# Kernel optimization log

Hardware: AMD Instinct MI355X
Metric: run time of the kernel (lower is better)

Reference implementation:

```python
import jax, jax.numpy as jnp
import numpy as np

B, S, D_IN, D_EMB = 16, 8192, 256, 256
LEVELS = 8  # pywt default max level for db1 with signal length 256: log2(256)
INV_SQRT2 = np.float32(1.0 / np.sqrt(2.0))


def haar_wavedec_concat(x, levels):
    """Multi-level Haar (db1) DWT along last axis; returns coeffs concatenated
    in pywt order [cA_L, cD_L, ..., cD_1]. Assumes last dim = 2**levels,
    so 'symmetric' padding is a no-op (filter length 2, even lengths).
    pywt db1 convention: cA[k]=(x[2k]+x[2k+1])/sqrt2, cD[k]=(x[2k]-x[2k+1])/sqrt2.
    """
    details = []
    a = x
    for _ in range(levels):
        even = a[..., ::2]
        odd = a[..., 1::2]
        details.append((even - odd) * INV_SQRT2)
        a = (even + odd) * INV_SQRT2
    return jnp.concatenate([a] + details[::-1], axis=-1)


def setup_inputs() -> dict:
    key = jax.random.key(0)
    k_x, k_w, k_b = jax.random.split(key, 3)
    x = jax.random.normal(k_x, (B, S, D_IN), dtype=jnp.float32)
    # nn.Linear(input_dim, embed_dim): W is (embed_dim, input_dim)
    bound = np.float32(1.0 / np.sqrt(D_IN))
    W = jax.random.uniform(k_w, (D_EMB, D_IN), dtype=jnp.float32, minval=-bound, maxval=bound)
    b = jax.random.uniform(k_b, (D_EMB,), dtype=jnp.float32, minval=-bound, maxval=bound)
    return {"x": x, "W": W, "b": b}


def reference(x, W, b):
    coeffs = haar_wavedec_concat(x, LEVELS)  # (B, S, D_IN)
    # concatenated coeff length == D_IN exactly, so no pad/trim (matches original no-op branch)
    return jnp.einsum('bsd,ed->bse', coeffs, W) + b
```

## Files before the change

### kernel.cpp

```cpp
#include <hip/hip_runtime.h>
#include <hip/hip_bf16.h>

typedef short short8 __attribute__((ext_vector_type(8)));
typedef float f32x4 __attribute__((ext_vector_type(4)));

#define INV_SQRT2F 0.70710678118654752440f

__device__ __forceinline__ unsigned short f2bf(float f) {
  union { float f; unsigned u; } v; v.f = f;
  unsigned u = v.u;
  unsigned r = (u + 0x7FFFu + ((u >> 16) & 1u)) >> 16;
  return (unsigned short)r;
}

__global__ void haar_pack(const float* __restrict__ W, unsigned short* __restrict__ Wp) {
  __shared__ float cbuf[4][256];
  __shared__ float buf0[4][256];
  __shared__ float buf1[4][256];
  const int tid = threadIdx.x;
  const int w = tid >> 6, l = tid & 63;
  const int e = blockIdx.x * 4 + w;
  const float* row = W + e * 256;
  for (int k = l; k < 256; k += 64) cbuf[w][k] = row[k];
  __syncthreads();
  if (l == 0) buf0[w][0] = cbuf[w][0];
  __syncthreads();
  float* A = buf0[w];
  float* Bv = buf1[w];
  int len = 1;
  for (int s = 0; s < 8; ++s) {
    for (int k = l; k < len; k += 64) {
      float av = A[k], dv = cbuf[w][len + k];
      Bv[2 * k]     = (av + dv) * INV_SQRT2F;
      Bv[2 * k + 1] = (av - dv) * INV_SQRT2F;
    }
    __syncthreads();
    float* t = A; A = Bv; Bv = t;
    len <<= 1;
  }
  const int nblk = e >> 4, lr = e & 15;
  for (int k = l; k < 256; k += 64) {
    int kk = k >> 5, win = k & 31, lhi = win >> 3, j = win & 7;
    int lane = lhi * 16 + lr;
    Wp[(((nblk * 8 + kk) * 64 + lane) << 3) + j] = f2bf(A[k]);
  }
}

#define NTILES 16
#define BM 32

#define BARRIER_LGKM() do { \
    __builtin_amdgcn_sched_barrier(0); \
    asm volatile("s_waitcnt lgkmcnt(0)" ::: "memory"); \
    __builtin_amdgcn_s_barrier(); \
    __builtin_amdgcn_sched_barrier(0); \
  } while (0)

__global__ __launch_bounds__(512, 1) void wemb_gemm(
    const float* __restrict__ x, const unsigned short* __restrict__ Wp,
    const float* __restrict__ bias, float* __restrict__ out) {
  __shared__ char al[2][16384];
  const int tid = threadIdx.x;
  const int w = tid >> 6, lane = tid & 63;
  const int wm = w >> 2, wn = w & 3;
  const int lr = lane & 15, lhi = lane >> 4;

  short8 Bf[8][4];
#pragma unroll
  for (int kk = 0; kk < 8; ++kk)
#pragma unroll
    for (int n = 0; n < 4; ++n)
      Bf[kk][n] = *(const short8*)(Wp + ((((wn * 4 + n) * 8 + kk) * 64 + lane) << 3));
#pragma unroll
  for (int kk = 0; kk < 8; ++kk)
#pragma unroll
    for (int n = 0; n < 4; ++n)
      asm volatile("" : "+v"(Bf[kk][n]));

  float bv[4];
#pragma unroll
  for (int n = 0; n < 4; ++n) bv[n] = bias[wn * 64 + n * 16 + lr];

  const long tile0 = (long)blockIdx.x * NTILES;
  float4 pfA[4], pfB[4];

  {
    const float4* s0 = (const float4*)(x + tile0 * (BM * 256));
    float4 t0[4];
#pragma unroll
    for (int i = 0; i < 4; ++i) t0[i] = s0[i * 512 + tid];
    const float4* s1 = (const float4*)(x + (tile0 + 1) * (BM * 256));
#pragma unroll
    for (int i = 0; i < 4; ++i) pfA[i] = s1[i * 512 + tid];
#pragma unroll
    for (int i = 0; i < 4; ++i) {
      int f = i * 512 + tid;
      int row = f >> 6, colb = (f & 63) * 8;
      ushort4 p;
      p.x = __bfloat16_as_ushort(__float2bfloat16(t0[i].x));
      p.y = __bfloat16_as_ushort(__float2bfloat16(t0[i].y));
      p.z = __bfloat16_as_ushort(__float2bfloat16(t0[i].z));
      p.w = __bfloat16_as_ushort(__float2bfloat16(t0[i].w));
      *(ushort4*)(al[0] + row * 512 + (colb ^ ((row & 7) << 4))) = p;
    }
  }
  BARRIER_LGKM();

#define STEP(IT, CUR, NXT, PFU, PFL)                                          \
  {                                                                           \
    const long tt = tile0 + (IT);                                             \
    if ((IT) + 2 < NTILES) {                                                  \
      const float4* src = (const float4*)(x + (tt + 2) * (BM * 256));         \
      _Pragma("unroll")                                                       \
      for (int i = 0; i < 4; ++i) PFL[i] = src[i * 512 + tid];                \
    }                                                                         \
    f32x4 acc[4];                                                             \
    _Pragma("unroll")                                                         \
    for (int n = 0; n < 4; ++n) acc[n] = (f32x4){0.f, 0.f, 0.f, 0.f};         \
    _Pragma("unroll")                                                         \
    for (int kk = 0; kk < 8; ++kk) {                                          \
      const int arow = wm * 16 + lr;                                          \
      const int colb = (kk * 32 + lhi * 8) * 2;                               \
      short8 a = *(const short8*)((CUR) + arow * 512 +                        \
                                  (colb ^ ((arow & 7) << 4)));                \
      _Pragma("unroll")                                                       \
      for (int n = 0; n < 4; ++n)                                             \
        acc[n] = __builtin_amdgcn_mfma_f32_16x16x32_bf16(a, Bf[kk][n],        \
                                                         acc[n], 0, 0, 0);    \
    }                                                                         \
    {                                                                         \
      float* orow = out + (tt * BM + wm * 16 + lhi * 4) * 256;                \
      _Pragma("unroll")                                                       \
      for (int n = 0; n < 4; ++n) {                                           \
        const int e = wn * 64 + n * 16 + lr;                                  \
        _Pragma("unroll")                                                     \
        for (int r = 0; r < 4; ++r) orow[r * 256 + e] = acc[n][r] + bv[n];    \
      }                                                                       \
    }                                                                         \
    if ((IT) + 1 < NTILES) {                                                  \
      _Pragma("unroll")                                                       \
      for (int i = 0; i < 4; ++i) {                                           \
        int f = i * 512 + tid;                                                \
        int row = f >> 6, colb = (f & 63) * 8;                                \
        ushort4 p;                                                            \
        p.x = __bfloat16_as_ushort(__float2bfloat16(PFU[i].x));               \
        p.y = __bfloat16_as_ushort(__float2bfloat16(PFU[i].y));               \
        p.z = __bfloat16_as_ushort(__float2bfloat16(PFU[i].z));               \
        p.w = __bfloat16_as_ushort(__float2bfloat16(PFU[i].w));               \
        *(ushort4*)((NXT) + row * 512 + (colb ^ ((row & 7) << 4))) = p;       \
      }                                                                       \
      BARRIER_LGKM();                                                         \
    }                                                                         \
  }

#pragma unroll 1
  for (int ip = 0; ip < NTILES / 2; ++ip) {
    const int it0 = ip * 2;
    STEP(it0,     al[0], al[1], pfA, pfB);
    STEP(it0 + 1, al[1], al[0], pfB, pfA);
  }
#undef STEP
}

extern "C" void kernel_launch(void* const* d_in, const int* in_sizes, int n_in,
                              void* d_out, int out_size, void* d_ws, size_t ws_size,
                              hipStream_t stream) {
  const float* x = (const float*)d_in[0];
  const float* W = (const float*)d_in[1];
  const float* b = (const float*)d_in[2];
  float* out = (float*)d_out;
  unsigned short* Wp = (unsigned short*)d_ws;

  haar_pack<<<64, 256, 0, stream>>>(W, Wp);

  const int grid = (out_size / 256) / (BM * NTILES);
  wemb_gemm<<<grid, 512, 0, stream>>>(x, Wp, b, out);
}
```

Before: 57.94 us.

## Compute Haar-transformed weights in closed form and double GEMM occupancy

The weight pre-transform kernel replaces the iterative shared-memory inverse-Haar loop with a direct closed-form sum per output element, one thread per element and one block per row, removing the barriers. The GEMM halves tiles per block (doubling grid size) and raises launch bounds to two blocks per CU, dropping the asm register pin on the B fragments. This aims to hide memory latency through more resident waves, at the risk of register pressure or spills from holding 32 B fragments under a tighter register budget.

```diff
diff --git a/kernel.cpp b/kernel.cpp
--- a/kernel.cpp
+++ b/kernel.cpp
@@ -3,8 +3,6 @@
 
 typedef short short8 __attribute__((ext_vector_type(8)));
 typedef float f32x4 __attribute__((ext_vector_type(4)));
-
-#define INV_SQRT2F 0.70710678118654752440f
 
 __device__ __forceinline__ unsigned short f2bf(float f) {
   union { float f; unsigned u; } v; v.f = f;
@@ -14,39 +12,26 @@
 }
 
 __global__ void haar_pack(const float* __restrict__ W, unsigned short* __restrict__ Wp) {
-  __shared__ float cbuf[4][256];
-  __shared__ float buf0[4][256];
-  __shared__ float buf1[4][256];
-  const int tid = threadIdx.x;
-  const int w = tid >> 6, l = tid & 63;
-  const int e = blockIdx.x * 4 + w;
+  const int e = blockIdx.x;
+  const int k = threadIdx.x;
   const float* row = W + e * 256;
-  for (int k = l; k < 256; k += 64) cbuf[w][k] = row[k];
-  __syncthreads();
-  if (l == 0) buf0[w][0] = cbuf[w][0];
-  __syncthreads();
-  float* A = buf0[w];
-  float* Bv = buf1[w];
-  int len = 1;
-  for (int s = 0; s < 8; ++s) {
-    for (int k = l; k < len; k += 64) {
-      float av = A[k], dv = cbuf[w][len + k];
-      Bv[2 * k]     = (av + dv) * INV_SQRT2F;
-      Bv[2 * k + 1] = (av - dv) * INV_SQRT2F;
-    }
-    __syncthreads();
-    float* t = A; A = Bv; Bv = t;
-    len <<= 1;
+  const float wgt[9] = {0.f,
+    0.70710678118654752f, 0.5f, 0.35355339059327376f, 0.25f,
+    0.17677669529663688f, 0.125f, 0.08838834764831844f, 0.0625f};
+  float acc = row[0] * 0.0625f;
+#pragma unroll
+  for (int l = 1; l <= 8; ++l) {
+    float g = wgt[l];
+    float s = ((k >> (l - 1)) & 1) ? -g : g;
+    acc += row[(1 << (8 - l)) + (k >> l)] * s;
   }
   const int nblk = e >> 4, lr = e & 15;
-  for (int k = l; k < 256; k += 64) {
-    int kk = k >> 5, win = k & 31, lhi = win >> 3, j = win & 7;
-    int lane = lhi * 16 + lr;
-    Wp[(((nblk * 8 + kk) * 64 + lane) << 3) + j] = f2bf(A[k]);
-  }
+  const int kk = k >> 5, win = k & 31, lhi = win >> 3, j = win & 7;
+  const int lane = lhi * 16 + lr;
+  Wp[(((nblk * 8 + kk) * 64 + lane) << 3) + j] = f2bf(acc);
 }
 
-#define NTILES 16
+#define NTILES 8
 #define BM 32
 
 #define BARRIER_LGKM() do { \
@@ -56,7 +41,7 @@
     __builtin_amdgcn_sched_barrier(0); \
   } while (0)
 
-__global__ __launch_bounds__(512, 1) void wemb_gemm(
+__global__ __launch_bounds__(512, 2) void wemb_gemm(
     const float* __restrict__ x, const unsigned short* __restrict__ Wp,
     const float* __restrict__ bias, float* __restrict__ out) {
   __shared__ char al[2][16384];
@@ -71,11 +56,6 @@
 #pragma unroll
     for (int n = 0; n < 4; ++n)
       Bf[kk][n] = *(const short8*)(Wp + ((((wn * 4 + n) * 8 + kk) * 64 + lane) << 3));
-#pragma unroll
-  for (int kk = 0; kk < 8; ++kk)
-#pragma unroll
-    for (int n = 0; n < 4; ++n)
-      asm volatile("" : "+v"(Bf[kk][n]));
 
   float bv[4];
 #pragma unroll
@@ -171,7 +151,7 @@
   float* out = (float*)d_out;
   unsigned short* Wp = (unsigned short*)d_ws;
 
-  haar_pack<<<64, 256, 0, stream>>>(W, Wp);
+  haar_pack<<<256, 256, 0, stream>>>(W, Wp);
 
   const int grid = (out_size / 256) / (BM * NTILES);
   wemb_gemm<<<grid, 512, 0, stream>>>(x, Wp, b, out);
```

Result: slower. 60.83 us (+5.0%).
